# Kernel tuning notes

Hardware: AMD Instinct MI355X
Metric: run time of the kernel (lower is better)

## Reference

```python
import jax, jax.numpy as jnp
import numpy as np

E, F, H = 8, 4096, 2048  # num_experts, ffn_hidden_size, hidden_size
B, S, K = 2, 1024, 4     # batch, seq_len, top_k


def setup_inputs() -> dict:
    key = jax.random.key(0)
    ks = jax.random.split(key, 7)
    x = jax.random.normal(ks[0], (B, S, H), dtype=jnp.float32)
    weights = jax.random.uniform(ks[1], (B * S, E), dtype=jnp.float32)
    top_weights = jax.random.uniform(ks[2], (B * S, K), dtype=jnp.float32)
    top_experts = jax.random.randint(ks[3], (B * S, K), 0, E)
    w1 = jax.random.normal(ks[4], (E, F, H), dtype=jnp.float32) * 0.02
    v1 = jax.random.normal(ks[5], (E, F, H), dtype=jnp.float32) * 0.02
    w2 = jax.random.normal(ks[6], (E, F, H), dtype=jnp.float32) * 0.02
    return {"x": x, "weights": weights, "top_weights": top_weights,
            "top_experts": top_experts, "w1": w1, "v1": v1, "w2": w2}


def reference(x, weights, top_weights, top_experts, w1, v1, w2):
    # weights (router probs) is accepted but unused, matching the torch forward.
    bsz, q_len, hidden = x.shape
    xt = x.reshape(-1, hidden)  # [T, H]
    num_experts = w1.shape[0]
    # scale[t, e] = sum_k top_weights[t, k] * (top_experts[t, k] == e)
    onehot = jax.nn.one_hot(top_experts, num_experts, dtype=xt.dtype)  # [T, K, E]
    scale = jnp.einsum("tke,tk->te", onehot, top_weights)  # [T, E]
    out = jnp.zeros_like(xt)
    for e in range(num_experts):  # fixed small expert loop, dense+masked combine
        gate = xt @ w1[e].T          # [T, F]
        up = xt @ v1[e].T            # [T, F]
        h = jax.nn.silu(gate) * up   # DbrxExpertGLU
        out = out + (h @ w2[e]) * scale[:, e:e + 1]
    return out.reshape(bsz, q_len, hidden)
```

## Files before the change

kernel.cpp:

```cpp
#include <hip/hip_runtime.h>
#include <hip/hip_bf16.h>

#define NE 8
#define FF 4096
#define HH 2048
#define TT 2048
#define KTOP 4

typedef unsigned short u16;
typedef __attribute__((ext_vector_type(8))) short bf16x8;
typedef __attribute__((ext_vector_type(4))) float f32x4;

__device__ __forceinline__ u16 f2u(float f) {
  __hip_bfloat16 b = __float2bfloat16(f);
  return *reinterpret_cast<u16*>(&b);
}

__device__ __forceinline__ void gld16(void* lds, const void* g) {
  __builtin_amdgcn_global_load_lds(
      (const __attribute__((address_space(1))) void*)g,
      (__attribute__((address_space(3))) void*)lds, 16, 0, 0);
}

__global__ void k_build(const int* __restrict__ te, int* __restrict__ cnt,
                        int* __restrict__ tok, int* __restrict__ posmap) {
  const int e = blockIdx.x;
  const int tl = threadIdx.x;
  const int base = tl * 8;
  int mem[8];
  int my = 0;
  #pragma unroll
  for (int i = 0; i < 8; ++i) {
    const int t = base + i;
    bool m = false;
    #pragma unroll
    for (int k = 0; k < KTOP; ++k) m |= (te[t * KTOP + k] == e);
    mem[i] = m ? 1 : 0;
    my += mem[i];
  }
  __shared__ int s[256];
  s[tl] = my;
  __syncthreads();
  for (int off = 1; off < 256; off <<= 1) {
    int v = (tl >= off) ? s[tl - off] : 0;
    __syncthreads();
    s[tl] += v;
    __syncthreads();
  }
  int r = s[tl] - my;
  if (tl == 255) cnt[e] = s[255];
  #pragma unroll
  for (int i = 0; i < 8; ++i) {
    if (mem[i]) {
      const int t = base + i;
      tok[e * TT + r] = t;
      posmap[t * NE + e] = r;
      ++r;
    }
  }
}

__global__ void k_cast4(const float4* __restrict__ src, ushort4* __restrict__ dst, int n4) {
  int stride = gridDim.x * blockDim.x;
  for (int i = blockIdx.x * blockDim.x + threadIdx.x; i < n4; i += stride) {
    float4 f = src[i];
    ushort4 o;
    o.x = f2u(f.x); o.y = f2u(f.y); o.z = f2u(f.z); o.w = f2u(f.w);
    dst[i] = o;
  }
}

__global__ void k_tcast(const float* __restrict__ w2, u16* __restrict__ dst) {
  const int e = blockIdx.z;
  const float* src = w2 + (size_t)e * FF * HH;
  u16* d = dst + (size_t)e * HH * FF;
  __shared__ float tile[32][33];
  int h0 = blockIdx.x * 32;
  int f0 = blockIdx.y * 32;
  int tx = threadIdx.x, ty = threadIdx.y;
  #pragma unroll
  for (int i = 0; i < 4; ++i)
    tile[ty + i*8][tx] = src[(size_t)(f0 + ty + i*8) * HH + h0 + tx];
  __syncthreads();
  #pragma unroll
  for (int i = 0; i < 4; ++i)
    d[(size_t)(h0 + ty + i*8) * FF + f0 + tx] = f2u(tile[tx][ty + i*8]);
}

__global__ void k_gather(const u16* __restrict__ xb, const int* __restrict__ tok,
                         const int* __restrict__ cnt, u16* __restrict__ xg) {
  const int e = blockIdx.y;
  const int r = blockIdx.x;
  const int c = cnt[e];
  const int mcap = (c + 255) & ~255;
  if (r >= mcap) return;
  uint4* dst = (uint4*)(xg + ((size_t)e * TT + r) * HH) + threadIdx.x;
  if (r < c) {
    const uint4* src = (const uint4*)(xb + (size_t)tok[e * TT + r] * HH) + threadIdx.x;
    *dst = *src;
  } else {
    *dst = (uint4){0, 0, 0, 0};
  }
}

template<int MODE>
__global__ __launch_bounds__(512)
void gemm256(const u16* __restrict__ Aall, const u16* __restrict__ Ball,
             const int* __restrict__ cnt, void* __restrict__ Oall,
             const float* __restrict__ W1, const float* __restrict__ V1) {
  constexpr int KD  = (MODE == 0) ? HH : FF;
  constexpr int NTK = KD / 64;
  constexpr int NT  = (MODE == 0) ? 32 : 8;
  constexpr int NB  = (MODE == 0) ? 2 * FF : HH;

  const int nwg = gridDim.x;
  const int bid = blockIdx.x;
  const int swz = (bid & 7) * (nwg >> 3) + (bid >> 3);
  const int e   = swz / (8 * NT);
  const int rem = swz % (8 * NT);
  const int ntl = rem / 8;
  const int mt  = rem % 8;
  const int c = cnt[e];
  const int mcap = (c + 255) & ~255;
  if (mt * 256 >= mcap) return;

  __shared__ __align__(16) u16 smem[65536];
  const int tid  = threadIdx.x;
  const int lane = tid & 63;
  const int wave = tid >> 6;
  const int wm = wave >> 2;
  const int wn = wave & 3;

  const u16* A = Aall + (size_t)e * TT * KD + (size_t)(mt * 256) * KD;

  const int tq = tid >> 2;
  const int tc = (((tid & 3) ^ ((tid >> 3) & 3)) << 3);
  const u16* pA = A + (size_t)tq * KD + tc;

  auto stageA = [&](int d, int ks, int kt) {
    u16* dst = smem + ((d * 2 + ks) << 13) + tid * 8;
    const u16* src = pA + kt * 64 + ks * 32;
    gld16(dst,        src);
    gld16(dst + 4096, src + (size_t)128 * KD);
  };

  const u16* pB = Ball + (size_t)e * NB * KD + (size_t)(ntl * 256) * KD
                       + (size_t)tq * KD + tc;
  auto stageB = [&](int d, int ks, int kt) {
    u16* dst = smem + 32768 + ((d * 2 + ks) << 13) + tid * 8;
    const u16* src = pB + kt * 64 + ks * 32;
    gld16(dst,        src);
    gld16(dst + 4096, src + (size_t)128 * KD);
  };

  const float* pW = nullptr;
  if constexpr (MODE == 0) {
    const int sel = (tq >> 4) & 1;
    const int fr  = ntl * 128 + (tq >> 5) * 16 + (tq & 15);
    pW = (sel ? V1 : W1) + ((size_t)(e * FF + fr)) * HH + (tid & 3) * 8;
  }
  float4 br0[4], br1[4];
  auto issueB = [&](float4* br, int ks, int kt) {
    const float* s = pW + kt * 64 + ks * 32;
    br[0] = ((const float4*)s)[0];
    br[1] = ((const float4*)s)[1];
    const float* s2 = s + (size_t)64 * HH;
    br[2] = ((const float4*)s2)[0];
    br[3] = ((const float4*)s2)[1];
  };
  auto cvtB = [&](float4* br, int d, int ks) {
    u16* dst = smem + 32768 + ((d * 2 + ks) << 13) + tq * 32 + tc;
    union { ushort u[8]; bf16x8 v; } lo, hi;
    lo.u[0]=f2u(br[0].x); lo.u[1]=f2u(br[0].y); lo.u[2]=f2u(br[0].z); lo.u[3]=f2u(br[0].w);
    lo.u[4]=f2u(br[1].x); lo.u[5]=f2u(br[1].y); lo.u[6]=f2u(br[1].z); lo.u[7]=f2u(br[1].w);
    hi.u[0]=f2u(br[2].x); hi.u[1]=f2u(br[2].y); hi.u[2]=f2u(br[2].z); hi.u[3]=f2u(br[2].w);
    hi.u[4]=f2u(br[3].x); hi.u[5]=f2u(br[3].y); hi.u[6]=f2u(br[3].z); hi.u[7]=f2u(br[3].w);
    *(bf16x8*)(dst)        = lo.v;
    *(bf16x8*)(dst + 4096) = hi.v;
  };

  f32x4 acc[8][4];
  #pragma unroll
  for (int m = 0; m < 8; ++m)
    #pragma unroll
    for (int n = 0; n < 4; ++n)
      acc[m][n] = (f32x4){0.f, 0.f, 0.f, 0.f};

  const int lr = lane & 15;
  const int lc = ((((lane >> 4) & 3) ^ ((lane >> 1) & 3)) << 3);

  bf16x8 af[4], bf[4];
  auto rdA = [&](int d, int ks, int mq) {
    const u16* blk = smem + ((d * 2 + ks) << 13);
    #pragma unroll
    for (int m = 0; m < 4; ++m)
      af[m] = *(const bf16x8*)(blk + (wm * 128 + mq * 64 + m * 16 + lr) * 32 + lc);
  };
  auto rdB = [&](int d, int ks) {
    const u16* blk = smem + 32768 + ((d * 2 + ks) << 13);
    #pragma unroll
    for (int n = 0; n < 4; ++n)
      bf[n] = *(const bf16x8*)(blk + (wn * 64 + n * 16 + lr) * 32 + lc);
  };
  auto vmwait = [&](int n) {
    switch (n) {
      case 0:  asm volatile("s_waitcnt vmcnt(0)"  ::: "memory"); break;
      case 2:  asm volatile("s_waitcnt vmcnt(2)"  ::: "memory"); break;
      case 4:  asm volatile("s_waitcnt vmcnt(4)"  ::: "memory"); break;
      case 6:  asm volatile("s_waitcnt vmcnt(6)"  ::: "memory"); break;
      default: asm volatile("s_waitcnt vmcnt(8)"  ::: "memory"); break;
    }
  };
  auto MF = [&](int mq) {
    __builtin_amdgcn_s_setprio(1);
    #pragma unroll
    for (int m = 0; m < 4; ++m)
      #pragma unroll
      for (int n = 0; n < 4; ++n)
        acc[mq * 4 + m][n] = __builtin_amdgcn_mfma_f32_16x16x32_bf16(
            af[m], bf[n], acc[mq * 4 + m][n], 0, 0, 0);
    __builtin_amdgcn_s_setprio(0);
  };

  if constexpr (MODE == 0) {
    issueB(br0, 0, 0);
    issueB(br1, 1, 0);
    stageA(0, 0, 0);
    stageA(0, 1, 0);
    cvtB(br0, 0, 0);
    cvtB(br1, 0, 1);
    issueB(br0, 0, 1);
    issueB(br1, 1, 1);
    vmwait(8);
    asm volatile("s_waitcnt lgkmcnt(0)" ::: "memory");
  } else {
    stageA(0, 0, 0); stageB(0, 0, 0);
    stageA(0, 1, 0); stageB(0, 1, 0);
    stageA(1, 0, 1);
    vmwait(6);
  }
  __builtin_amdgcn_s_barrier();

  for (int t = 0; t < NTK; ++t) {
    const int d = t & 1, dn = d ^ 1;
    const bool hasN  = (t + 1 < NTK);
    const bool hasN2 = (t + 2 < NTK);
    rdB(d, 0); rdA(d, 0, 0);
    if constexpr (MODE == 0) { if (hasN) stageA(dn, 0, t + 1); }
    else                     { if (hasN) stageB(dn, 0, t + 1); }
    __builtin_amdgcn_s_barrier();
    asm volatile("s_waitcnt lgkmcnt(0)" ::: "memory");
    __builtin_amdgcn_sched_barrier(0);
    MF(0);
    __builtin_amdgcn_s_barrier();
    rdA(d, 0, 1);
    if (hasN) stageA(dn, 1, t + 1);
    __builtin_amdgcn_s_barrier();
    asm volatile("s_waitcnt lgkmcnt(0)" ::: "memory");
    __builtin_amdgcn_sched_barrier(0);
    MF(1);
    if constexpr (MODE == 1) {
      int v = 4 * NTK - 4 * t - 4; v = v > 3 ? 3 : (v < 0 ? 0 : v);
      vmwait(v * 2);
    }
    __builtin_amdgcn_s_barrier();
    rdB(d, 1); rdA(d, 1, 0);
    if constexpr (MODE == 0) {
      if (hasN)  cvtB(br0, dn, 0);
      if (hasN2) issueB(br0, 0, t + 2);
    } else {
      if (hasN) stageB(dn, 1, t + 1);
    }
    __builtin_amdgcn_s_barrier();
    asm volatile("s_waitcnt lgkmcnt(0)" ::: "memory");
    __builtin_amdgcn_sched_barrier(0);
    MF(0);
    __builtin_amdgcn_s_barrier();
    rdA(d, 1, 1);
    if constexpr (MODE == 0) {
      if (hasN)  cvtB(br1, dn, 1);
      if (hasN2) issueB(br1, 1, t + 2);
    } else {
      if (hasN2) stageA(d, 0, t + 2);
    }
    __builtin_amdgcn_s_barrier();
    asm volatile("s_waitcnt lgkmcnt(0)" ::: "memory");
    __builtin_amdgcn_sched_barrier(0);
    MF(1);
    if constexpr (MODE == 0) {
      vmwait(hasN2 ? 8 : 0);
    } else {
      int v = 4 * NTK - 4 * t - 6; v = v > 3 ? 3 : (v < 0 ? 0 : v);
      vmwait(v * 2);
    }
    __builtin_amdgcn_s_barrier();
  }

  const int rb = mt * 256 + wm * 128 + ((lane >> 4) << 2);
  if (MODE == 0) {
    u16* H = (u16*)Oall + (size_t)e * TT * FF;
    const int fb = ntl * 128 + wn * 32 + lr;
    #pragma unroll
    for (int m = 0; m < 8; ++m)
      #pragma unroll
      for (int np = 0; np < 2; ++np)
        #pragma unroll
        for (int j = 0; j < 4; ++j) {
          float g = acc[m][2*np][j];
          float u = acc[m][2*np + 1][j];
          float hh = (g / (1.f + __expf(-g))) * u;
          H[(size_t)(rb + m*16 + j) * FF + fb + np*16] = f2u(hh);
        }
  } else {
    float* D = (float*)Oall + (size_t)e * TT * HH;
    const int cb = ntl * 256 + wn * 64 + lr;
    #pragma unroll
    for (int m = 0; m < 8; ++m)
      #pragma unroll
      for (int n = 0; n < 4; ++n)
        #pragma unroll
        for (int j = 0; j < 4; ++j)
          D[(size_t)(rb + m*16 + j) * HH + cb + n*16] = acc[m][n][j];
  }
}

__global__ void k_combine(const float* __restrict__ tw, const int* __restrict__ te,
                          const int* __restrict__ posmap, const float* __restrict__ dcomp,
                          float* __restrict__ out) {
  const int t = blockIdx.x;
  const int c0 = threadIdx.x * 8;
  float a[8] = {0.f, 0.f, 0.f, 0.f, 0.f, 0.f, 0.f, 0.f};
  #pragma unroll
  for (int k = 0; k < KTOP; ++k) {
    const int e = te[t * KTOP + k];
    const float w = tw[t * KTOP + k];
    const int r = posmap[t * NE + e];
    const float* row = dcomp + ((size_t)e * TT + r) * HH + c0;
    const float4 p = ((const float4*)row)[0];
    const float4 q = ((const float4*)row)[1];
    a[0] += w * p.x; a[1] += w * p.y; a[2] += w * p.z; a[3] += w * p.w;
    a[4] += w * q.x; a[5] += w * q.y; a[6] += w * q.z; a[7] += w * q.w;
  }
  float* o = out + (size_t)t * HH + c0;
  ((float4*)o)[0] = (float4){a[0], a[1], a[2], a[3]};
  ((float4*)o)[1] = (float4){a[4], a[5], a[6], a[7]};
}

extern "C" void kernel_launch(void* const* d_in, const int* in_sizes, int n_in,
                              void* d_out, int out_size, void* d_ws, size_t ws_size,
                              hipStream_t stream) {
  const float* x  = (const float*)d_in[0];
  const float* tw = (const float*)d_in[2];
  const int*   te = (const int*)d_in[3];
  const float* w1 = (const float*)d_in[4];
  const float* v1 = (const float*)d_in[5];
  const float* w2 = (const float*)d_in[6];
  float* out = (float*)d_out;

  char* p = (char*)d_ws;
  int*   cnt    = (int*)p;   p += 256;
  int*   tok    = (int*)p;   p += (size_t)NE * TT * 4;
  int*   posmap = (int*)p;   p += (size_t)TT * NE * 4;
  u16*   xb     = (u16*)p;   p += (size_t)TT * HH * 2;
  u16*   xg     = (u16*)p;   p += (size_t)NE * TT * HH * 2;
  u16*   w2tb   = (u16*)p;   p += (size_t)NE * HH * FF * 2;
  u16*   hc     = (u16*)p;   p += (size_t)NE * TT * FF * 2;
  float* dcomp  = (float*)p; p += (size_t)NE * TT * HH * 4;

  k_build<<<NE, 256, 0, stream>>>(te, cnt, tok, posmap);
  k_cast4<<<1024, 256, 0, stream>>>((const float4*)x, (ushort4*)xb, TT * HH / 4);
  k_tcast<<<dim3(HH / 32, FF / 32, NE), dim3(32, 8), 0, stream>>>(w2, w2tb);
  k_gather<<<dim3(TT, NE), 256, 0, stream>>>(xb, tok, cnt, xg);

  gemm256<0><<<2048, 512, 0, stream>>>(xg, w2tb, cnt, hc, w1, v1);
  gemm256<1><<<512, 512, 0, stream>>>(hc, w2tb, cnt, dcomp, nullptr, nullptr);
  k_combine<<<TT, 256, 0, stream>>>(tw, te, posmap, dcomp, out);
}
```

Before: 538.2 us.

## Fuse token gather into first GEMM A-loads, widen w2 transpose tile

Removes the separate gather kernel and gathered x buffer: the first GEMM now loads A rows directly from the bf16 x via per-row token indices, using a zeroed pad row for rows past the expert count. The w2 transpose-cast kernel processes 64-row tiles and writes ushort2 pairs for wider stores. The MODE 0 B-conversion/issue steps are reordered to occur after the MFMA blocks in the pipeline. This saves a kernel launch and a large write/read of gathered activations, at the cost of indirect per-row global addressing in the GEMM.

```diff
diff --git a/kernel.cpp b/kernel.cpp
--- a/kernel.cpp
+++ b/kernel.cpp
@@ -74,32 +74,21 @@
   const int e = blockIdx.z;
   const float* src = w2 + (size_t)e * FF * HH;
   u16* d = dst + (size_t)e * HH * FF;
-  __shared__ float tile[32][33];
+  __shared__ float tile[64][33];
   int h0 = blockIdx.x * 32;
-  int f0 = blockIdx.y * 32;
+  int f0 = blockIdx.y * 64;
   int tx = threadIdx.x, ty = threadIdx.y;
   #pragma unroll
-  for (int i = 0; i < 4; ++i)
-    tile[ty + i*8][tx] = src[(size_t)(f0 + ty + i*8) * HH + h0 + tx];
+  for (int i = 0; i < 8; ++i)
+    tile[ty + i * 8][tx] = src[(size_t)(f0 + ty + i * 8) * HH + h0 + tx];
   __syncthreads();
   #pragma unroll
-  for (int i = 0; i < 4; ++i)
-    d[(size_t)(h0 + ty + i*8) * FF + f0 + tx] = f2u(tile[tx][ty + i*8]);
-}
-
-__global__ void k_gather(const u16* __restrict__ xb, const int* __restrict__ tok,
-                         const int* __restrict__ cnt, u16* __restrict__ xg) {
-  const int e = blockIdx.y;
-  const int r = blockIdx.x;
-  const int c = cnt[e];
-  const int mcap = (c + 255) & ~255;
-  if (r >= mcap) return;
-  uint4* dst = (uint4*)(xg + ((size_t)e * TT + r) * HH) + threadIdx.x;
-  if (r < c) {
-    const uint4* src = (const uint4*)(xb + (size_t)tok[e * TT + r] * HH) + threadIdx.x;
-    *dst = *src;
-  } else {
-    *dst = (uint4){0, 0, 0, 0};
+  for (int i = 0; i < 4; ++i) {
+    const int hh = ty + i * 8;
+    ushort2 o;
+    o.x = f2u(tile[tx * 2][hh]);
+    o.y = f2u(tile[tx * 2 + 1][hh]);
+    *(ushort2*)&d[(size_t)(h0 + hh) * FF + f0 + tx * 2] = o;
   }
 }
 
@@ -107,7 +96,8 @@
 __global__ __launch_bounds__(512)
 void gemm256(const u16* __restrict__ Aall, const u16* __restrict__ Ball,
              const int* __restrict__ cnt, void* __restrict__ Oall,
-             const float* __restrict__ W1, const float* __restrict__ V1) {
+             const float* __restrict__ W1, const float* __restrict__ V1,
+             const int* __restrict__ tok, const u16* __restrict__ Zp) {
   constexpr int KD  = (MODE == 0) ? HH : FF;
   constexpr int NTK = KD / 64;
   constexpr int NT  = (MODE == 0) ? 32 : 8;
@@ -131,17 +121,27 @@
   const int wm = wave >> 2;
   const int wn = wave & 3;
 
-  const u16* A = Aall + (size_t)e * TT * KD + (size_t)(mt * 256) * KD;
-
   const int tq = tid >> 2;
   const int tc = (((tid & 3) ^ ((tid >> 3) & 3)) << 3);
-  const u16* pA = A + (size_t)tq * KD + tc;
+
+  const u16* pA0;
+  const u16* pA1;
+  if constexpr (MODE == 0) {
+    const int r0 = mt * 256 + tq;
+    const int r1 = r0 + 128;
+    pA0 = ((r0 < c) ? Aall + (size_t)tok[e * TT + r0] * HH : Zp) + tc;
+    pA1 = ((r1 < c) ? Aall + (size_t)tok[e * TT + r1] * HH : Zp) + tc;
+  } else {
+    const u16* A = Aall + (size_t)e * TT * KD + (size_t)(mt * 256) * KD;
+    pA0 = A + (size_t)tq * KD + tc;
+    pA1 = pA0 + (size_t)128 * KD;
+  }
 
   auto stageA = [&](int d, int ks, int kt) {
     u16* dst = smem + ((d * 2 + ks) << 13) + tid * 8;
-    const u16* src = pA + kt * 64 + ks * 32;
-    gld16(dst,        src);
-    gld16(dst + 4096, src + (size_t)128 * KD);
+    const int off = kt * 64 + ks * 32;
+    gld16(dst,        pA0 + off);
+    gld16(dst + 4096, pA1 + off);
   };
 
   const u16* pB = Ball + (size_t)e * NB * KD + (size_t)(ntl * 256) * KD
@@ -265,29 +265,25 @@
     }
     __builtin_amdgcn_s_barrier();
     rdB(d, 1); rdA(d, 1, 0);
+    if constexpr (MODE == 1) { if (hasN) stageB(dn, 1, t + 1); }
+    __builtin_amdgcn_s_barrier();
+    asm volatile("s_waitcnt lgkmcnt(0)" ::: "memory");
+    __builtin_amdgcn_sched_barrier(0);
+    MF(0);
     if constexpr (MODE == 0) {
       if (hasN)  cvtB(br0, dn, 0);
       if (hasN2) issueB(br0, 0, t + 2);
-    } else {
-      if (hasN) stageB(dn, 1, t + 1);
-    }
+    }
+    __builtin_amdgcn_s_barrier();
+    rdA(d, 1, 1);
+    if constexpr (MODE == 1) { if (hasN2) stageA(d, 0, t + 2); }
     __builtin_amdgcn_s_barrier();
     asm volatile("s_waitcnt lgkmcnt(0)" ::: "memory");
     __builtin_amdgcn_sched_barrier(0);
-    MF(0);
-    __builtin_amdgcn_s_barrier();
-    rdA(d, 1, 1);
+    MF(1);
     if constexpr (MODE == 0) {
       if (hasN)  cvtB(br1, dn, 1);
       if (hasN2) issueB(br1, 1, t + 2);
-    } else {
-      if (hasN2) stageA(d, 0, t + 2);
-    }
-    __builtin_amdgcn_s_barrier();
-    asm volatile("s_waitcnt lgkmcnt(0)" ::: "memory");
-    __builtin_amdgcn_sched_barrier(0);
-    MF(1);
-    if constexpr (MODE == 0) {
       vmwait(hasN2 ? 8 : 0);
     } else {
       int v = 4 * NTK - 4 * t - 6; v = v > 3 ? 3 : (v < 0 ? 0 : v);
@@ -361,18 +357,19 @@
   int*   cnt    = (int*)p;   p += 256;
   int*   tok    = (int*)p;   p += (size_t)NE * TT * 4;
   int*   posmap = (int*)p;   p += (size_t)TT * NE * 4;
+  u16*   zp     = (u16*)p;   p += (size_t)HH * 2;
   u16*   xb     = (u16*)p;   p += (size_t)TT * HH * 2;
-  u16*   xg     = (u16*)p;   p += (size_t)NE * TT * HH * 2;
   u16*   w2tb   = (u16*)p;   p += (size_t)NE * HH * FF * 2;
   u16*   hc     = (u16*)p;   p += (size_t)NE * TT * FF * 2;
   float* dcomp  = (float*)p; p += (size_t)NE * TT * HH * 4;
 
+  hipMemsetAsync(zp, 0, (size_t)HH * 2, stream);
   k_build<<<NE, 256, 0, stream>>>(te, cnt, tok, posmap);
   k_cast4<<<1024, 256, 0, stream>>>((const float4*)x, (ushort4*)xb, TT * HH / 4);
-  k_tcast<<<dim3(HH / 32, FF / 32, NE), dim3(32, 8), 0, stream>>>(w2, w2tb);
-  k_gather<<<dim3(TT, NE), 256, 0, stream>>>(xb, tok, cnt, xg);
-
-  gemm256<0><<<2048, 512, 0, stream>>>(xg, w2tb, cnt, hc, w1, v1);
-  gemm256<1><<<512, 512, 0, stream>>>(hc, w2tb, cnt, dcomp, nullptr, nullptr);
+  k_tcast<<<dim3(HH / 32, FF / 64, NE), dim3(32, 8), 0, stream>>>(w2, w2tb);
+
+  gemm256<0><<<2048, 512, 0, stream>>>(xb, w2tb, cnt, hc, w1, v1, tok, zp);
+  gemm256<1><<<512, 512, 0, stream>>>(hc, w2tb, cnt, dcomp, nullptr, nullptr,
+                                      nullptr, nullptr);
   k_combine<<<TT, 256, 0, stream>>>(tw, te, posmap, dcomp, out);
 }
```

Result: slower. 550.5 us (+2.3%).
